# Performance work log

Measured on AMD Instinct MI355X. Metric: run time of the kernel, lower is better.

## Reference

```python
import jax, jax.numpy as jnp
import numpy as np

VOCAB = 65
N_EMBED = 384
BLOCK = 256
N_HEAD = 6
HEAD_SIZE = 4  # forward uses sa_heads = MultiHeadAttention(4), NOT the Block stack
B, T = 128, 256


def setup_inputs() -> dict:
    key = jax.random.key(0)
    ks = jax.random.split(key, 16)
    s = lambda *sh: 0.02
    inp = {
        "idx": jax.random.randint(ks[0], (B, T), 0, VOCAB),
        "targets": jax.random.randint(ks[1], (B, T), 0, VOCAB),
        "tok_emb": jax.random.normal(ks[2], (VOCAB, N_EMBED), jnp.float32) * 0.02,
        "pos_emb": jax.random.normal(ks[3], (BLOCK, N_EMBED), jnp.float32) * 0.02,
        "Wq": jax.random.normal(ks[4], (N_HEAD, N_EMBED, HEAD_SIZE), jnp.float32) * 0.05,
        "Wk": jax.random.normal(ks[5], (N_HEAD, N_EMBED, HEAD_SIZE), jnp.float32) * 0.05,
        "Wv": jax.random.normal(ks[6], (N_HEAD, N_EMBED, HEAD_SIZE), jnp.float32) * 0.05,
        "Wproj": jax.random.normal(ks[7], (N_HEAD * HEAD_SIZE, N_EMBED), jnp.float32) * 0.05,
        "bproj": jnp.zeros((N_EMBED,), jnp.float32),
        "W1": jax.random.normal(ks[8], (N_EMBED, 4 * N_EMBED), jnp.float32) * 0.02,
        "b1": jnp.zeros((4 * N_EMBED,), jnp.float32),
        "W2": jax.random.normal(ks[9], (4 * N_EMBED, N_EMBED), jnp.float32) * 0.02,
        "b2": jnp.zeros((N_EMBED,), jnp.float32),
        "Wlm": jax.random.normal(ks[10], (N_EMBED, VOCAB), jnp.float32) * 0.02,
        "blm": jnp.zeros((VOCAB,), jnp.float32),
    }
    return inp


def _forward(idx, targets, tok_emb, pos_emb, Wq, Wk, Wv, Wproj, bproj, W1, b1, W2, b2, Wlm, blm):
    Bb, Tt = idx.shape
    x = tok_emb[idx] + pos_emb[:Tt]  # [B,T,C]
    # multi-head attention (manual, causal). NOTE: source scales by n_embed**-0.5 (C of input), not head_size.
    q = jnp.einsum("btc,hcd->bhtd", x, Wq)
    k = jnp.einsum("btc,hcd->bhtd", x, Wk)
    v = jnp.einsum("btc,hcd->bhtd", x, Wv)
    scores = jnp.einsum("bhtd,bhsd->bhts", q, k) * (N_EMBED ** -0.5)
    causal = jnp.tril(jnp.ones((Tt, Tt), bool))
    scores = jnp.where(causal, scores, -jnp.inf)
    w = jax.nn.softmax(scores, axis=-1)  # dropout = identity in eval
    attn = jnp.einsum("bhts,bhsd->bhtd", w, v)
    attn = attn.transpose(0, 2, 1, 3).reshape(Bb, Tt, N_HEAD * HEAD_SIZE)
    x = attn @ Wproj + bproj
    # feed-forward
    x = jax.nn.relu(x @ W1 + b1) @ W2 + b2
    logits = x @ Wlm + blm  # [B,T,V]
    logits_flat = logits.reshape(Bb * Tt, VOCAB)
    t_flat = targets.reshape(Bb * Tt)
    logp = jax.nn.log_softmax(logits_flat, axis=-1)
    loss = -jnp.mean(jnp.take_along_axis(logp, t_flat[:, None], axis=1))
    return logits_flat, loss


def reference(idx, targets, tok_emb, pos_emb, Wq, Wk, Wv, Wproj, bproj, W1, b1, W2, b2, Wlm, blm):
    return _forward(idx, targets, tok_emb, pos_emb, Wq, Wk, Wv, Wproj, bproj, W1, b1, W2, b2, Wlm, blm)
```

## Files before the change

### kernel.cpp

```cpp
#include <hip/hip_runtime.h>
#include <hip/hip_bf16.h>
#include <math.h>

typedef __hip_bfloat16 bf16;
typedef __attribute__((ext_vector_type(8))) short bf16x8;
typedef __attribute__((ext_vector_type(4))) float f32x4;
typedef __attribute__((ext_vector_type(8))) int i32x8;
typedef __attribute__((ext_vector_type(4))) int i32x4;
typedef unsigned char u8;
typedef unsigned int u32;

#define T_SEQ   256
#define C_EMB   384
#define NH      6
#define HS      4
#define NB      128
#define NTOK    (NB * T_SEQ)
#define VOC     65
#define FFDIM   1536
#define QKVW    72
#define PROJK   32
#define XROWS   (VOC * T_SEQ)

#define X2_SCALE    128.0f
#define W1_SCALE    128.0f
#define FF1_DESCALE (1.0f / (128.0f * 128.0f))
#define H1_SCALE    512.0f
#define W2_SCALE    128.0f
#define FF2_DESCALE (1.0f / (512.0f * 128.0f))

__device__ __forceinline__ float bf2f(bf16 x) { return __bfloat162float(x); }
__device__ __forceinline__ bf16  f2b(float x) { return __float2bfloat16(x); }
__device__ __forceinline__ short f2s(float x) { bf16 b = __float2bfloat16(x); return *reinterpret_cast<short*>(&b); }
__device__ __forceinline__ u8 f2fp8(float x) {
    return (u8)(__builtin_amdgcn_cvt_pk_fp8_f32(x, x, 0, false) & 0xff);
}
__device__ __forceinline__ u32 pk4fp8(const float* w) {
    int p = __builtin_amdgcn_cvt_pk_fp8_f32(w[0], w[1], 0, false);
    p = __builtin_amdgcn_cvt_pk_fp8_f32(w[2], w[3], p, true);
    return (u32)p;
}

__device__ __forceinline__ void glds16(const void* g, void* l) {
    __builtin_amdgcn_global_load_lds((const __attribute__((address_space(1))) void*)g,
                                     (__attribute__((address_space(3))) void*)l, 16, 0, 0);
}

__global__ void pack_all_kernel(const float* __restrict__ Wq, const float* __restrict__ Wk,
                                const float* __restrict__ Wv, const float* __restrict__ Wlm,
                                const float* __restrict__ Wproj,
                                const float* __restrict__ W1, const float* __restrict__ W2,
                                const float* __restrict__ tok_emb, const float* __restrict__ pos_emb,
                                bf16* __restrict__ WqkvT, bf16* __restrict__ WlmT,
                                bf16* __restrict__ WprojT, u8* __restrict__ W1P,
                                u8* __restrict__ W2P, bf16* __restrict__ xtab,
                                float* __restrict__ lossbuf) {
    int blk = blockIdx.x;
    int t = threadIdx.x;
    if (blk == 0 && t == 0) { lossbuf[0] = 0.f; ((int*)lossbuf)[1] = 0; }
    if (blk < 128) {
        int n = blk;
        for (int c = t; c < C_EMB; c += 256) {
            float v = 0.f;
            if (n < QKVW) {
                int sel = n / 24, r = n % 24, h = r >> 2, d = r & 3;
                const float* W = (sel == 0) ? Wq : (sel == 1) ? Wk : Wv;
                v = W[(h * C_EMB + c) * HS + d];
            }
            WqkvT[(size_t)n * C_EMB + c] = f2b(v);
        }
    } else if (blk < 256) {
        int n = blk - 128;
        for (int c = t; c < C_EMB; c += 256)
            WlmT[(size_t)n * C_EMB + c] = f2b(n < VOC ? Wlm[(size_t)c * VOC + n] : 0.f);
    } else if (blk < 640) {
        int n = blk - 256;
        int k = t;
        if (k < PROJK)
            WprojT[(size_t)n * PROJK + k] = f2b(k < 24 ? Wproj[(size_t)k * C_EMB + n] : 0.f);
    } else if (blk < 640 + 288) {
        int fb = blk - 640;
        int n16 = fb / 3, kk = fb % 3;
        int b0 = t * 8;
        int l = b0 >> 5;
        int j0 = b0 & 31;
        int n = n16 * 16 + (l & 15);
        int kb = kk * 128 + (l >> 4) * 32 + j0;
        union { u8 b[8]; uint2 u; } pk;
        #pragma unroll
        for (int e = 0; e < 8; ++e)
            pk.b[e] = f2fp8(W1[(size_t)(kb + e) * FFDIM + n] * W1_SCALE);
        *(uint2*)&W1P[(size_t)fb * 2048 + b0] = pk.u;
    } else if (blk < 640 + 576) {
        int fb = blk - 640 - 288;
        int n16 = fb / 12, kc = fb % 12;
        int b0 = t * 8;
        int l = b0 >> 5;
        int j0 = b0 & 31;
        int n = n16 * 16 + (l & 15);
        int kb = kc * 128 + (l >> 4) * 32 + j0;
        union { u8 b[8]; uint2 u; } pk;
        #pragma unroll
        for (int e = 0; e < 8; ++e)
            pk.b[e] = f2fp8(W2[(size_t)(kb + e) * C_EMB + n] * W2_SCALE);
        *(uint2*)&W2P[(size_t)fb * 2048 + b0] = pk.u;
    } else {
        int base = (blk - (640 + 576)) * 4;
        for (int r = 0; r < 4; ++r) {
            int row = base + r;
            int id = row >> 8, tt = row & 255;
            const float* te = tok_emb + (size_t)id * C_EMB;
            const float* pe = pos_emb + (size_t)tt * C_EMB;
            bf16* dst = xtab + (size_t)row * C_EMB;
            for (int c = t; c < C_EMB; c += 256)
                dst[c] = f2b(te[c] + pe[c]);
        }
    }
}

__global__ __launch_bounds__(512)
void qkv_gather_kernel(const int* __restrict__ idx, const bf16* __restrict__ xtab,
                       const bf16* __restrict__ Bt, float* __restrict__ outf) {
    __shared__ __align__(16) u8 As[16384];
    __shared__ __align__(16) u8 Bs[16384];
    __shared__ int rowid[128];
    int tid = threadIdx.x, lane = tid & 63, wave = tid >> 6;
    int bm = blockIdx.x * 128;
    int wm = (wave & 1) * 64, wn = (wave >> 1) * 32;
    int lrow = lane & 15, kq = lane >> 4;
    if (tid < 128) { int token = bm + tid; rowid[tid] = idx[token] * T_SEQ + (token & (T_SEQ - 1)); }
    __syncthreads();

    int r0 = tid >> 3;
    int s0 = (((tid & 7) * 16) - (r0 & 7) * 16) & 127;
    int c1 = tid + 512;
    int r1 = c1 >> 3;
    int s1 = (((c1 & 7) * 16) - (r1 & 7) * 16) & 127;
    const u8* xb = (const u8*)xtab;
    const u8* bb = (const u8*)Bt;
    long gA0 = (long)rowid[r0] * 768 + s0;
    long gA1 = (long)rowid[r1] * 768 + s1;
    long gB0 = (long)r0 * 768 + s0;
    long gB1 = (long)r1 * 768 + s1;
    int ro = (lrow & 7) * 16;

    f32x4 acc[4][2] = {};
    for (int k0 = 0; k0 < 768; k0 += 128) {
        glds16(xb + gA0 + k0, As + (size_t)tid * 16);
        glds16(xb + gA1 + k0, As + (size_t)c1 * 16);
        glds16(bb + gB0 + k0, Bs + (size_t)tid * 16);
        glds16(bb + gB1 + k0, Bs + (size_t)c1 * 16);
        __syncthreads();
        #pragma unroll
        for (int ks = 0; ks < 2; ++ks) {
            int off = (ks * 64 + kq * 16 + ro) & 127;
            bf16x8 af[4], bff[2];
            #pragma unroll
            for (int i = 0; i < 4; ++i)
                af[i] = *(const bf16x8*)&As[(size_t)(wm + i * 16 + lrow) * 128 + off];
            #pragma unroll
            for (int i = 0; i < 2; ++i)
                bff[i] = *(const bf16x8*)&Bs[(size_t)(wn + i * 16 + lrow) * 128 + off];
            #pragma unroll
            for (int mi = 0; mi < 4; ++mi)
                #pragma unroll
                for (int ni = 0; ni < 2; ++ni)
                    acc[mi][ni] = __builtin_amdgcn_mfma_f32_16x16x32_bf16(af[mi], bff[ni], acc[mi][ni], 0, 0, 0);
        }
        __syncthreads();
    }

    #pragma unroll
    for (int ni = 0; ni < 2; ++ni) {
        int col = wn + ni * 16 + lrow;
        if (col >= QKVW) continue;
        #pragma unroll
        for (int mi = 0; mi < 4; ++mi) {
            int orow = bm + wm + mi * 16 + kq * 4;
            #pragma unroll
            for (int r = 0; r < 4; ++r)
                outf[(size_t)(orow + r) * QKVW + col] = acc[mi][ni][r];
        }
    }
}

__global__ void attn_kernel(const float* __restrict__ qkv,
                            bf16* __restrict__ attnT) {
    int bh = blockIdx.x;
    int b = bh / NH, h = bh % NH;
    int t = threadIdx.x;
    __shared__ float4 kv[T_SEQ][2];
    const float* base = qkv + (size_t)(b * T_SEQ) * QKVW;
    kv[t][0] = *(const float4*)(base + t * QKVW + 24 + h * HS);
    kv[t][1] = *(const float4*)(base + t * QKVW + 48 + h * HS);
    __syncthreads();
    const float scale = 0.05103103630798288f;
    float4 q = *(const float4*)(base + t * QKVW + h * HS);
    float qx = q.x * scale, qy = q.y * scale, qz = q.z * scale, qw = q.w * scale;
    float sum0 = 0.f, sum1 = 0.f;
    float o0x = 0.f, o0y = 0.f, o0z = 0.f, o0w = 0.f;
    float o1x = 0.f, o1y = 0.f, o1z = 0.f, o1w = 0.f;
    int s = 0;
    for (; s + 1 <= t; s += 2) {
        float4 k0 = kv[s][0],     v0 = kv[s][1];
        float4 k1 = kv[s + 1][0], v1 = kv[s + 1][1];
        float p0 = __expf(qx * k0.x + qy * k0.y + qz * k0.z + qw * k0.w);
        float p1 = __expf(qx * k1.x + qy * k1.y + qz * k1.z + qw * k1.w);
        sum0 += p0; sum1 += p1;
        o0x += p0 * v0.x; o0y += p0 * v0.y; o0z += p0 * v0.z; o0w += p0 * v0.w;
        o1x += p1 * v1.x; o1y += p1 * v1.y; o1z += p1 * v1.z; o1w += p1 * v1.w;
    }
    if (s <= t) {
        float4 k0 = kv[s][0], v0 = kv[s][1];
        float p0 = __expf(qx * k0.x + qy * k0.y + qz * k0.z + qw * k0.w);
        sum0 += p0;
        o0x += p0 * v0.x; o0y += p0 * v0.y; o0z += p0 * v0.z; o0w += p0 * v0.w;
    }
    float inv = 1.f / (sum0 + sum1);
    bf16* out = attnT + (size_t)(b * T_SEQ + t) * PROJK + h * HS;
    out[0] = f2b((o0x + o1x) * inv);
    out[1] = f2b((o0y + o1y) * inv);
    out[2] = f2b((o0z + o1z) * inv);
    out[3] = f2b((o0w + o1w) * inv);
    if (h == 0) {
        bf16* pad = attnT + (size_t)(b * T_SEQ + t) * PROJK + 24;
        *(uint4*)pad = uint4{0, 0, 0, 0};
    }
}

__global__ __launch_bounds__(1024, 4)
void ff_mega_kernel(const bf16* __restrict__ attnT, const bf16* __restrict__ WprojT,
                    const float* __restrict__ bproj,
                    const u8* __restrict__ W1P, const float* __restrict__ b1,
                    const u8* __restrict__ W2P, const float* __restrict__ b2,
                    bf16* __restrict__ x3) {
    __shared__ __align__(16) u8 smem[98304];
    u8* x2_lds = smem;
    u8* h1t    = smem + 49152;
    short* As_p = (short*)(smem + 49152);
    short* Bs_p = (short*)(smem + 57344);

    int tid  = threadIdx.x;
    int lane = tid & 63;
    int wave = tid >> 6;
    int wrow = wave & 3;
    int wcol = wave >> 2;
    int bm   = blockIdx.x * 128;
    int lrow  = lane & 15;
    int khalf = lane >> 4;
    int wm  = wrow * 32;
    int wn6 = wcol * 96;
    int wn4 = wcol * 64;

    if (tid < 512) {
        int row = tid >> 2;
        int i0 = (tid & 3) * 16;
        int selem = ((i0 - ((row >> 1) & 3) * 16) & 63) >> 1;
        glds16(attnT + (size_t)(bm + row) * PROJK + selem, As_p + (size_t)tid * 8);
    }
    {
        int rowb = tid >> 2;
        int sel2 = (((tid & 3) * 16 - ((rowb >> 1) & 3) * 16) & 63) >> 1;
        glds16(WprojT + (size_t)rowb * PROJK + sel2, Bs_p + (size_t)tid * 8);
        int c = tid + 1024;
        if (c < 1536) {
            int rb = c >> 2;
            int s2 = (((c & 3) * 16 - ((rb >> 1) & 3) * 16) & 63) >> 1;
            glds16(WprojT + (size_t)rb * PROJK + s2, Bs_p + (size_t)c * 8);
        }
    }
    __syncthreads();

    f32x4 accp[2][6] = {};
    {
        int arot16 = ((lrow >> 1) & 3) * 16;
        int roff = ((khalf * 16 + arot16) & 63) >> 1;
        bf16x8 afp[2], bfp[6];
        #pragma unroll
        for (int i = 0; i < 2; ++i)
            afp[i] = *(const bf16x8*)&As_p[(size_t)(wm + i * 16 + lrow) * 32 + roff];
        #pragma unroll
        for (int i = 0; i < 6; ++i)
            bfp[i] = *(const bf16x8*)&Bs_p[(size_t)(wn6 + i * 16 + lrow) * 32 + roff];
        #pragma unroll
        for (int mi = 0; mi < 2; ++mi)
            #pragma unroll
            for (int ni = 0; ni < 6; ++ni)
                accp[mi][ni] = __builtin_amdgcn_mfma_f32_16x16x32_bf16(bfp[ni], afp[mi], accp[mi][ni], 0, 0, 0);
    }

    #pragma unroll
    for (int mi = 0; mi < 2; ++mi) {
        int m = wm + mi * 16 + lrow;
        #pragma unroll
        for (int ni = 0; ni < 6; ++ni) {
            int n0 = wn6 + ni * 16 + khalf * 4;
            float4 bv = *(const float4*)(bproj + n0);
            float w[4];
            w[0] = (accp[mi][ni][0] + bv.x) * X2_SCALE;
            w[1] = (accp[mi][ni][1] + bv.y) * X2_SCALE;
            w[2] = (accp[mi][ni][2] + bv.z) * X2_SCALE;
            w[3] = (accp[mi][ni][3] + bv.w) * X2_SCALE;
            *(u32*)&x2_lds[(size_t)(n0 >> 7) * 16384 + (size_t)m * 128 +
                           (((n0 & 127) + (m & 7) * 16) & 127)] = pk4fp8(w);
        }
    }
    __syncthreads();

    int arot8 = (lrow & 7) * 16;
    int off0 = (khalf * 32 + arot8) & 127;
    int off1 = (off0 + 16) & 127;

    f32x4 acc1[2][4] = {};
    f32x4 acc2[2][6] = {};

    for (int nt = 0; nt < 6; ++nt) {
        #pragma unroll
        for (int kk = 0; kk < 3; ++kk) {
            const u8* abase = x2_lds + (size_t)kk * 16384;
            i32x8 a[2];
            #pragma unroll
            for (int i = 0; i < 2; ++i) {
                const u8* rp = abase + (size_t)(wm + i * 16 + lrow) * 128;
                i32x4 lo = *(const i32x4*)(rp + off0);
                i32x4 hi = *(const i32x4*)(rp + off1);
                a[i][0]=lo[0]; a[i][1]=lo[1]; a[i][2]=lo[2]; a[i][3]=lo[3];
                a[i][4]=hi[0]; a[i][5]=hi[1]; a[i][6]=hi[2]; a[i][7]=hi[3];
            }
            const u8* wbase = W1P + ((size_t)((nt * 16 + wcol * 4) * 3 + kk)) * 2048
                                  + (size_t)lane * 32;
            #pragma unroll
            for (int j = 0; j < 4; ++j) {
                const u8* p = wbase + (size_t)j * 3 * 2048;
                i32x4 lo = *(const i32x4*)p;
                i32x4 hi = *(const i32x4*)(p + 16);
                i32x8 b;
                b[0]=lo[0]; b[1]=lo[1]; b[2]=lo[2]; b[3]=lo[3];
                b[4]=hi[0]; b[5]=hi[1]; b[6]=hi[2]; b[7]=hi[3];
                #pragma unroll
                for (int mi = 0; mi < 2; ++mi)
                    acc1[mi][j] = __builtin_amdgcn_mfma_scale_f32_16x16x128_f8f6f4(
                        b, a[mi], acc1[mi][j], 0, 0,
                        0, 0x7f7f7f7f, 0, 0x7f7f7f7f);
            }
        }

        #pragma unroll
        for (int mi = 0; mi < 2; ++mi) {
            int m = wm + mi * 16 + lrow;
            #pragma unroll
            for (int ni = 0; ni < 4; ++ni) {
                int n0 = wn4 + ni * 16 + khalf * 4;
                float4 bv = *(const float4*)(b1 + nt * 256 + n0);
                float w[4];
                w[0] = fmaxf(acc1[mi][ni][0] * FF1_DESCALE + bv.x, 0.f) * H1_SCALE;
                w[1] = fmaxf(acc1[mi][ni][1] * FF1_DESCALE + bv.y, 0.f) * H1_SCALE;
                w[2] = fmaxf(acc1[mi][ni][2] * FF1_DESCALE + bv.z, 0.f) * H1_SCALE;
                w[3] = fmaxf(acc1[mi][ni][3] * FF1_DESCALE + bv.w, 0.f) * H1_SCALE;
                *(u32*)&h1t[(size_t)m * 256 + ((n0 + (m & 7) * 16) & 255)] = pk4fp8(w);
                acc1[mi][ni] = f32x4{0.f, 0.f, 0.f, 0.f};
            }
        }
        __syncthreads();

        #pragma unroll
        for (int sk = 0; sk < 2; ++sk) {
            i32x8 a2[2];
            #pragma unroll
            for (int i = 0; i < 2; ++i) {
                const u8* rp = h1t + (size_t)(wm + i * 16 + lrow) * 256;
                int o0 = (sk * 128 + khalf * 32 + arot8) & 255;
                int o1 = (sk * 128 + khalf * 32 + 16 + arot8) & 255;
                i32x4 lo = *(const i32x4*)(rp + o0);
                i32x4 hi = *(const i32x4*)(rp + o1);
                a2[i][0]=lo[0]; a2[i][1]=lo[1]; a2[i][2]=lo[2]; a2[i][3]=lo[3];
                a2[i][4]=hi[0]; a2[i][5]=hi[1]; a2[i][6]=hi[2]; a2[i][7]=hi[3];
            }
            int kc = nt * 2 + sk;
            #pragma unroll
            for (int half = 0; half < 2; ++half) {
                #pragma unroll
                for (int j = 0; j < 3; ++j) {
                    int n16 = wcol * 6 + half * 3 + j;
                    const u8* p = W2P + ((size_t)n16 * 12 + kc) * 2048 + (size_t)lane * 32;
                    i32x4 lo = *(const i32x4*)p;
                    i32x4 hi = *(const i32x4*)(p + 16);
                    i32x8 bw;
                    bw[0]=lo[0]; bw[1]=lo[1]; bw[2]=lo[2]; bw[3]=lo[3];
                    bw[4]=hi[0]; bw[5]=hi[1]; bw[6]=hi[2]; bw[7]=hi[3];
                    #pragma unroll
                    for (int mi = 0; mi < 2; ++mi)
                        acc2[mi][half * 3 + j] = __builtin_amdgcn_mfma_scale_f32_16x16x128_f8f6f4(
                            bw, a2[mi], acc2[mi][half * 3 + j], 0, 0,
                            0, 0x7f7f7f7f, 0, 0x7f7f7f7f);
                }
            }
        }
        __syncthreads();
    }

    u8* Ep = smem;
    #pragma unroll
    for (int mi = 0; mi < 2; ++mi) {
        int m = wm + mi * 16 + lrow;
        #pragma unroll
        for (int ni = 0; ni < 6; ++ni) {
            int n0 = wn6 + ni * 16 + khalf * 4;
            float4 bv = *(const float4*)(b2 + n0);
            union { short s[4]; uint2 u; } pk;
            pk.s[0] = f2s(acc2[mi][ni][0] * FF2_DESCALE + bv.x);
            pk.s[1] = f2s(acc2[mi][ni][1] * FF2_DESCALE + bv.y);
            pk.s[2] = f2s(acc2[mi][ni][2] * FF2_DESCALE + bv.z);
            pk.s[3] = f2s(acc2[mi][ni][3] * FF2_DESCALE + bv.w);
            *(uint2*)&Ep[(size_t)m * 768 + ((n0 >> 7) << 8) +
                         ((((n0 & 127) * 2) + (m & 7) * 16) & 255)] = pk.u;
        }
    }
    __syncthreads();
    #pragma unroll
    for (int p = 0; p < 6; ++p) {
        int c = tid + p * 1024;
        int row = c / 48;
        int sl = c - row * 48;
        int g0 = sl * 16;
        int chunk = g0 >> 8;
        int loc = g0 & 255;
        uint4 v = *(const uint4*)&Ep[(size_t)row * 768 + (chunk << 8) +
                                     ((loc + (row & 7) * 16) & 255)];
        *(uint4*)((u8*)x3 + (size_t)(bm + row) * 768 + g0) = v;
    }
}

__global__ __launch_bounds__(512)
void lm_loss_kernel(const bf16* __restrict__ A, const bf16* __restrict__ Bt,
                    const float* __restrict__ bias, const int* __restrict__ targets,
                    float* __restrict__ outf, float* __restrict__ lossbuf,
                    float* __restrict__ out_loss, int M, int K) {
    __shared__ short As[128][32];
    __shared__ short Bs[128][32];
    __shared__ float Ls[128][66];
    __shared__ float red[128];
    int tid  = threadIdx.x;
    int lane = tid & 63;
    int wave = tid >> 6;
    int bm = blockIdx.x * 128;
    int wm = (wave & 1) * 64;
    int wn = (wave >> 1) * 32;
    int lrow  = lane & 15;
    int khalf = lane >> 4;

    int row = tid >> 2;
    int i0 = (tid & 3) * 16;
    int selem = ((i0 - ((row >> 1) & 3) * 16) & 63) >> 1;
    int arot = ((lrow >> 1) & 3) * 16;
    int roff = ((khalf * 16 + arot) & 63) >> 1;

    f32x4 acc[4][2] = {};
    for (int k0 = 0; k0 < K; k0 += 32) {
        glds16(A  + (size_t)(bm + row) * K + k0 + selem, (short*)As + (size_t)tid * 8);
        glds16(Bt + (size_t)row * K + k0 + selem,        (short*)Bs + (size_t)tid * 8);
        __syncthreads();

        bf16x8 af[4], bff[2];
        #pragma unroll
        for (int i = 0; i < 4; ++i)
            af[i] = *(const bf16x8*)&As[wm + i * 16 + lrow][roff];
        #pragma unroll
        for (int i = 0; i < 2; ++i)
            bff[i] = *(const bf16x8*)&Bs[wn + i * 16 + lrow][roff];
        #pragma unroll
        for (int mi = 0; mi < 4; ++mi)
            #pragma unroll
            for (int ni = 0; ni < 2; ++ni)
                acc[mi][ni] = __builtin_amdgcn_mfma_f32_16x16x32_bf16(af[mi], bff[ni], acc[mi][ni], 0, 0, 0);
        __syncthreads();
    }

    #pragma unroll
    for (int ni = 0; ni < 2; ++ni) {
        int col = wn + ni * 16 + lrow;
        if (col >= VOC) continue;
        float bv = bias[col];
        #pragma unroll
        for (int mi = 0; mi < 4; ++mi) {
            int lr = wm + mi * 16 + khalf * 4;
            #pragma unroll
            for (int r = 0; r < 4; ++r) {
                float v = acc[mi][ni][r] + bv;
                outf[(size_t)(bm + lr + r) * VOC + col] = v;
                Ls[lr + r][col] = v;
            }
        }
    }
    __syncthreads();

    if (tid < 128) {
        int token = bm + tid;
        int tgt = targets[token];
        float m = -1e30f, s = 0.f;
        #pragma unroll 8
        for (int c = 0; c < VOC; ++c) {
            float v = Ls[tid][c];
            float mn = fmaxf(m, v);
            s = s * __expf(m - mn) + __expf(v - mn);
            m = mn;
        }
        red[tid] = m + logf(s) - Ls[tid][tgt];
    }
    __syncthreads();
    if (tid < 64) {
        float s = red[tid] + red[tid + 64];
        #pragma unroll
        for (int off = 32; off > 0; off >>= 1) s += __shfl_xor(s, off);
        if (tid == 0) {
            atomicAdd(&lossbuf[0], s);
            __threadfence();
            int done = atomicAdd(&((int*)lossbuf)[1], 1);
            if (done == (NTOK / 128) - 1) {
                __threadfence();
                float total = atomicAdd(&lossbuf[0], 0.0f);
                out_loss[0] = total / (float)NTOK;
            }
        }
    }
}

extern "C" void kernel_launch(void* const* d_in, const int* in_sizes, int n_in,
                              void* d_out, int out_size, void* d_ws, size_t ws_size,
                              hipStream_t stream) {
    const int*   idx     = (const int*)  d_in[0];
    const int*   targets = (const int*)  d_in[1];
    const float* tok_emb = (const float*)d_in[2];
    const float* pos_emb = (const float*)d_in[3];
    const float* Wq      = (const float*)d_in[4];
    const float* Wk      = (const float*)d_in[5];
    const float* Wv      = (const float*)d_in[6];
    const float* Wproj   = (const float*)d_in[7];
    const float* bproj   = (const float*)d_in[8];
    const float* W1      = (const float*)d_in[9];
    const float* b1      = (const float*)d_in[10];
    const float* W2      = (const float*)d_in[11];
    const float* b2      = (const float*)d_in[12];
    const float* Wlm     = (const float*)d_in[13];
    const float* blm     = (const float*)d_in[14];

    char* ws = (char*)d_ws;
    bf16*  WprojT = (bf16*) (ws + 0);
    float* qkvbuf = (float*)(ws + 25165824);
    bf16*  attnT  = (bf16*) (ws + 34603008);
    bf16*  xtab   = (bf16*) (ws + 37748736);
    bf16*  x3     = (bf16*) (ws + 163577856);
    float* lossbuf= (float*)(ws + 188743680);
    u8*    W1P    = (u8*)   (ws + 188874752);
    u8*    W2P    = (u8*)   (ws + 190054400);
    bf16*  WqkvT  = (bf16*) (ws + 191234048);
    bf16*  WlmT   = (bf16*) (ws + 191332352);

    float* out_logits = (float*)d_out;
    float* out_loss   = out_logits + (size_t)NTOK * VOC;

    pack_all_kernel<<<640 + 576 + XROWS / 4, 256, 0, stream>>>(
        Wq, Wk, Wv, Wlm, Wproj, W1, W2, tok_emb, pos_emb,
        WqkvT, WlmT, WprojT, W1P, W2P, xtab, lossbuf);

    qkv_gather_kernel<<<NTOK / 128, 512, 0, stream>>>(idx, xtab, WqkvT, qkvbuf);
    attn_kernel<<<NB * NH, T_SEQ, 0, stream>>>(qkvbuf, attnT);

    ff_mega_kernel<<<NTOK / 128, 1024, 0, stream>>>(attnT, WprojT, bproj,
                                                    W1P, b1, W2P, b2, x3);

    lm_loss_kernel<<<NTOK / 128, 512, 0, stream>>>(x3, WlmT, blm, targets,
                                                   out_logits, lossbuf, out_loss, NTOK, C_EMB);
}
```

Measured before the change: 243.2 us.

## Halve row tiles in QKV and FF kernels, widen lm_loss K-tile

```diff
diff --git a/kernel.cpp b/kernel.cpp
--- a/kernel.cpp
+++ b/kernel.cpp
@@ -105,7 +105,7 @@
             pk.b[e] = f2fp8(W2[(size_t)(kb + e) * C_EMB + n] * W2_SCALE);
         *(uint2*)&W2P[(size_t)fb * 2048 + b0] = pk.u;
     } else {
-        int base = (blk - (640 + 576)) * 4;
+        int base = (blk - 1216) * 4;
         for (int r = 0; r < 4; ++r) {
             int row = base + r;
             int id = row >> 8, tt = row & 255;
@@ -121,14 +121,14 @@
 __global__ __launch_bounds__(512)
 void qkv_gather_kernel(const int* __restrict__ idx, const bf16* __restrict__ xtab,
                        const bf16* __restrict__ Bt, float* __restrict__ outf) {
-    __shared__ __align__(16) u8 As[16384];
+    __shared__ __align__(16) u8 As[8192];
     __shared__ __align__(16) u8 Bs[16384];
-    __shared__ int rowid[128];
+    __shared__ int rowid[64];
     int tid = threadIdx.x, lane = tid & 63, wave = tid >> 6;
-    int bm = blockIdx.x * 128;
-    int wm = (wave & 1) * 64, wn = (wave >> 1) * 32;
+    int bm = blockIdx.x * 64;
+    int wm = (wave & 1) * 32, wn = (wave >> 1) * 32;
     int lrow = lane & 15, kq = lane >> 4;
-    if (tid < 128) { int token = bm + tid; rowid[tid] = idx[token] * T_SEQ + (token & (T_SEQ - 1)); }
+    if (tid < 64) { int token = bm + tid; rowid[tid] = idx[token] * T_SEQ + (token & (T_SEQ - 1)); }
     __syncthreads();
 
     int r0 = tid >> 3;
@@ -139,30 +139,28 @@
     const u8* xb = (const u8*)xtab;
     const u8* bb = (const u8*)Bt;
     long gA0 = (long)rowid[r0] * 768 + s0;
-    long gA1 = (long)rowid[r1] * 768 + s1;
     long gB0 = (long)r0 * 768 + s0;
     long gB1 = (long)r1 * 768 + s1;
     int ro = (lrow & 7) * 16;
 
-    f32x4 acc[4][2] = {};
+    f32x4 acc[2][2] = {};
     for (int k0 = 0; k0 < 768; k0 += 128) {
         glds16(xb + gA0 + k0, As + (size_t)tid * 16);
-        glds16(xb + gA1 + k0, As + (size_t)c1 * 16);
         glds16(bb + gB0 + k0, Bs + (size_t)tid * 16);
         glds16(bb + gB1 + k0, Bs + (size_t)c1 * 16);
         __syncthreads();
         #pragma unroll
         for (int ks = 0; ks < 2; ++ks) {
             int off = (ks * 64 + kq * 16 + ro) & 127;
-            bf16x8 af[4], bff[2];
-            #pragma unroll
-            for (int i = 0; i < 4; ++i)
+            bf16x8 af[2], bff[2];
+            #pragma unroll
+            for (int i = 0; i < 2; ++i)
                 af[i] = *(const bf16x8*)&As[(size_t)(wm + i * 16 + lrow) * 128 + off];
             #pragma unroll
             for (int i = 0; i < 2; ++i)
                 bff[i] = *(const bf16x8*)&Bs[(size_t)(wn + i * 16 + lrow) * 128 + off];
             #pragma unroll
-            for (int mi = 0; mi < 4; ++mi)
+            for (int mi = 0; mi < 2; ++mi)
                 #pragma unroll
                 for (int ni = 0; ni < 2; ++ni)
                     acc[mi][ni] = __builtin_amdgcn_mfma_f32_16x16x32_bf16(af[mi], bff[ni], acc[mi][ni], 0, 0, 0);
@@ -175,7 +173,7 @@
         int col = wn + ni * 16 + lrow;
         if (col >= QKVW) continue;
         #pragma unroll
-        for (int mi = 0; mi < 4; ++mi) {
+        for (int mi = 0; mi < 2; ++mi) {
             int orow = bm + wm + mi * 16 + kq * 4;
             #pragma unroll
             for (int r = 0; r < 4; ++r)
@@ -228,81 +226,56 @@
     }
 }
 
-__global__ __launch_bounds__(1024, 4)
+__global__ __launch_bounds__(512, 4)
 void ff_mega_kernel(const bf16* __restrict__ attnT, const bf16* __restrict__ WprojT,
                     const float* __restrict__ bproj,
                     const u8* __restrict__ W1P, const float* __restrict__ b1,
                     const u8* __restrict__ W2P, const float* __restrict__ b2,
                     bf16* __restrict__ x3) {
-    __shared__ __align__(16) u8 smem[98304];
+    __shared__ __align__(16) u8 smem[49152];
     u8* x2_lds = smem;
-    u8* h1t    = smem + 49152;
-    short* As_p = (short*)(smem + 49152);
-    short* Bs_p = (short*)(smem + 57344);
+    u8* h1t    = smem + 24576;
 
     int tid  = threadIdx.x;
     int lane = tid & 63;
     int wave = tid >> 6;
-    int wrow = wave & 3;
-    int wcol = wave >> 2;
-    int bm   = blockIdx.x * 128;
+    int bm   = blockIdx.x * 64;
     int lrow  = lane & 15;
     int khalf = lane >> 4;
-    int wm  = wrow * 32;
-    int wn6 = wcol * 96;
-    int wn4 = wcol * 64;
-
-    if (tid < 512) {
-        int row = tid >> 2;
-        int i0 = (tid & 3) * 16;
-        int selem = ((i0 - ((row >> 1) & 3) * 16) & 63) >> 1;
-        glds16(attnT + (size_t)(bm + row) * PROJK + selem, As_p + (size_t)tid * 8);
-    }
-    {
-        int rowb = tid >> 2;
-        int sel2 = (((tid & 3) * 16 - ((rowb >> 1) & 3) * 16) & 63) >> 1;
-        glds16(WprojT + (size_t)rowb * PROJK + sel2, Bs_p + (size_t)tid * 8);
-        int c = tid + 1024;
-        if (c < 1536) {
-            int rb = c >> 2;
-            int s2 = (((c & 3) * 16 - ((rb >> 1) & 3) * 16) & 63) >> 1;
-            glds16(WprojT + (size_t)rb * PROJK + s2, Bs_p + (size_t)c * 8);
-        }
-    }
-    __syncthreads();
-
-    f32x4 accp[2][6] = {};
-    {
-        int arot16 = ((lrow >> 1) & 3) * 16;
-        int roff = ((khalf * 16 + arot16) & 63) >> 1;
-        bf16x8 afp[2], bfp[6];
+    int wmh = (wave & 1) * 32;
+    int wn6 = (wave >> 1) * 96;
+    int wc  = wave >> 1;
+
+    #pragma unroll
+    for (int ph = 0; ph < 2; ++ph) {
+        f32x4 accp[2][3] = {};
+        bf16x8 afp[2], bfp[3];
         #pragma unroll
         for (int i = 0; i < 2; ++i)
-            afp[i] = *(const bf16x8*)&As_p[(size_t)(wm + i * 16 + lrow) * 32 + roff];
-        #pragma unroll
-        for (int i = 0; i < 6; ++i)
-            bfp[i] = *(const bf16x8*)&Bs_p[(size_t)(wn6 + i * 16 + lrow) * 32 + roff];
+            afp[i] = *(const bf16x8*)&attnT[(size_t)(bm + wmh + i * 16 + lrow) * PROJK + khalf * 8];
+        #pragma unroll
+        for (int i = 0; i < 3; ++i)
+            bfp[i] = *(const bf16x8*)&WprojT[(size_t)(wn6 + (ph * 3 + i) * 16 + lrow) * PROJK + khalf * 8];
         #pragma unroll
         for (int mi = 0; mi < 2; ++mi)
             #pragma unroll
-            for (int ni = 0; ni < 6; ++ni)
+            for (int ni = 0; ni < 3; ++ni)
                 accp[mi][ni] = __builtin_amdgcn_mfma_f32_16x16x32_bf16(bfp[ni], afp[mi], accp[mi][ni], 0, 0, 0);
-    }
-
-    #pragma unroll
-    for (int mi = 0; mi < 2; ++mi) {
-        int m = wm + mi * 16 + lrow;
-        #pragma unroll
-        for (int ni = 0; ni < 6; ++ni) {
-            int n0 = wn6 + ni * 16 + khalf * 4;
-            float4 bv = *(const float4*)(bproj + n0);
-            float w[4];
-            w[0] = (accp[mi][ni][0] + bv.x) * X2_SCALE;
-            w[1] = (accp[mi][ni][1] + bv.y) * X2_SCALE;
-            w[2] = (accp[mi][ni][2] + bv.z) * X2_SCALE;
-            w[3] = (accp[mi][ni][3] + bv.w) * X2_SCALE;
-            *(u32*)&x2_lds[(size_t)(n0 >> 7) * 16384 + (size_t)m * 128 +
-                           (((n0 & 127) + (m & 7) * 16) & 127)] = pk4fp8(w);
+        #pragma unroll
+        for (int mi = 0; mi < 2; ++mi) {
+            int m = wmh + mi * 16 + lrow;
+            #pragma unroll
+            for (int ni = 0; ni < 3; ++ni) {
+                int n0 = wn6 + (ph * 3 + ni) * 16 + khalf * 4;
+                float4 bv = *(const float4*)(bproj + n0);
+                float w[4];
+                w[0] = (accp[mi][ni][0] + bv.x) * X2_SCALE;
+                w[1] = (accp[mi][ni][1] + bv.y) * X2_SCALE;
+                w[2] = (accp[mi][ni][2] + bv.z) * X2_SCALE;
+                w[3] = (accp[mi][ni][3] + bv.w) * X2_SCALE;
+                *(u32*)&x2_lds[(size_t)(n0 >> 7) * 8192 + (size_t)m * 128 +
+                               (((n0 & 127) + (m & 7) * 16) & 127)] = pk4fp8(w);
+            }
         }
     }
     __syncthreads();
@@ -311,23 +284,23 @@
     int off0 = (khalf * 32 + arot8) & 127;
     int off1 = (off0 + 16) & 127;
 
-    f32x4 acc1[2][4] = {};
     f32x4 acc2[2][6] = {};
 
     for (int nt = 0; nt < 6; ++nt) {
+        f32x4 acc1[2][4] = {};
         #pragma unroll
         for (int kk = 0; kk < 3; ++kk) {
-            const u8* abase = x2_lds + (size_t)kk * 16384;
+            const u8* abase = x2_lds + (size_t)kk * 8192;
             i32x8 a[2];
             #pragma unroll
             for (int i = 0; i < 2; ++i) {
-                const u8* rp = abase + (size_t)(wm + i * 16 + lrow) * 128;
+                const u8* rp = abase + (size_t)(wmh + i * 16 + lrow) * 128;
                 i32x4 lo = *(const i32x4*)(rp + off0);
                 i32x4 hi = *(const i32x4*)(rp + off1);
                 a[i][0]=lo[0]; a[i][1]=lo[1]; a[i][2]=lo[2]; a[i][3]=lo[3];
                 a[i][4]=hi[0]; a[i][5]=hi[1]; a[i][6]=hi[2]; a[i][7]=hi[3];
             }
-            const u8* wbase = W1P + ((size_t)((nt * 16 + wcol * 4) * 3 + kk)) * 2048
+            const u8* wbase = W1P + ((size_t)((nt * 16 + wc * 4) * 3 + kk)) * 2048
                                   + (size_t)lane * 32;
             #pragma unroll
             for (int j = 0; j < 4; ++j) {
@@ -347,10 +320,10 @@
 
         #pragma unroll
         for (int mi = 0; mi < 2; ++mi) {
-            int m = wm + mi * 16 + lrow;
+            int m = wmh + mi * 16 + lrow;
             #pragma unroll
             for (int ni = 0; ni < 4; ++ni) {
-                int n0 = wn4 + ni * 16 + khalf * 4;
+                int n0 = wc * 64 + ni * 16 + khalf * 4;
                 float4 bv = *(const float4*)(b1 + nt * 256 + n0);
                 float w[4];
                 w[0] = fmaxf(acc1[mi][ni][0] * FF1_DESCALE + bv.x, 0.f) * H1_SCALE;
@@ -358,7 +331,6 @@
                 w[2] = fmaxf(acc1[mi][ni][2] * FF1_DESCALE + bv.z, 0.f) * H1_SCALE;
                 w[3] = fmaxf(acc1[mi][ni][3] * FF1_DESCALE + bv.w, 0.f) * H1_SCALE;
                 *(u32*)&h1t[(size_t)m * 256 + ((n0 + (m & 7) * 16) & 255)] = pk4fp8(w);
-                acc1[mi][ni] = f32x4{0.f, 0.f, 0.f, 0.f};
             }
         }
         __syncthreads();
@@ -368,7 +340,7 @@
             i32x8 a2[2];
             #pragma unroll
             for (int i = 0; i < 2; ++i) {
-                const u8* rp = h1t + (size_t)(wm + i * 16 + lrow) * 256;
+                const u8* rp = h1t + (size_t)(wmh + i * 16 + lrow) * 256;
                 int o0 = (sk * 128 + khalf * 32 + arot8) & 255;
                 int o1 = (sk * 128 + khalf * 32 + 16 + arot8) & 255;
                 i32x4 lo = *(const i32x4*)(rp + o0);
@@ -381,7 +353,7 @@
             for (int half = 0; half < 2; ++half) {
                 #pragma unroll
                 for (int j = 0; j < 3; ++j) {
-                    int n16 = wcol * 6 + half * 3 + j;
+                    int n16 = (wave >> 1) * 6 + half * 3 + j;
                     const u8* p = W2P + ((size_t)n16 * 12 + kc) * 2048 + (size_t)lane * 32;
                     i32x4 lo = *(const i32x4*)p;
                     i32x4 hi = *(const i32x4*)(p + 16);
@@ -402,7 +374,7 @@
     u8* Ep = smem;
     #pragma unroll
     for (int mi = 0; mi < 2; ++mi) {
-        int m = wm + mi * 16 + lrow;
+        int m = wmh + mi * 16 + lrow;
         #pragma unroll
         for (int ni = 0; ni < 6; ++ni) {
             int n0 = wn6 + ni * 16 + khalf * 4;
@@ -419,7 +391,7 @@
     __syncthreads();
     #pragma unroll
     for (int p = 0; p < 6; ++p) {
-        int c = tid + p * 1024;
+        int c = tid + p * 512;
         int row = c / 48;
         int sl = c - row * 48;
         int g0 = sl * 16;
@@ -435,9 +407,9 @@
 void lm_loss_kernel(const bf16* __restrict__ A, const bf16* __restrict__ Bt,
                     const float* __restrict__ bias, const int* __restrict__ targets,
                     float* __restrict__ outf, float* __restrict__ lossbuf,
-                    float* __restrict__ out_loss, int M, int K) {
-    __shared__ short As[128][32];
-    __shared__ short Bs[128][32];
+                    float* __restrict__ out_loss) {
+    __shared__ __align__(16) u8 As[16384];
+    __shared__ __align__(16) u8 Bs[16384];
     __shared__ float Ls[128][66];
     __shared__ float red[128];
     int tid  = threadIdx.x;
@@ -449,30 +421,42 @@
     int lrow  = lane & 15;
     int khalf = lane >> 4;
 
-    int row = tid >> 2;
-    int i0 = (tid & 3) * 16;
-    int selem = ((i0 - ((row >> 1) & 3) * 16) & 63) >> 1;
-    int arot = ((lrow >> 1) & 3) * 16;
-    int roff = ((khalf * 16 + arot) & 63) >> 1;
+    int r0 = tid >> 3;
+    int s0 = (((tid & 7) * 16) - (r0 & 7) * 16) & 127;
+    int c1 = tid + 512;
+    int r1 = c1 >> 3;
+    int s1 = (((c1 & 7) * 16) - (r1 & 7) * 16) & 127;
+    const u8* ab = (const u8*)A;
+    const u8* bb = (const u8*)Bt;
+    long gA0 = (long)(bm + r0) * 768 + s0;
+    long gA1 = (long)(bm + r1) * 768 + s1;
+    long gB0 = (long)r0 * 768 + s0;
+    long gB1 = (long)r1 * 768 + s1;
+    int ro = (lrow & 7) * 16;
 
     f32x4 acc[4][2] = {};
-    for (int k0 = 0; k0 < K; k0 += 32) {
-        glds16(A  + (size_t)(bm + row) * K + k0 + selem, (short*)As + (size_t)tid * 8);
-        glds16(Bt + (size_t)row * K + k0 + selem,        (short*)Bs + (size_t)tid * 8);
+    for (int k0 = 0; k0 < 768; k0 += 128) {
+        glds16(ab + gA0 + k0, As + (size_t)tid * 16);
+        glds16(ab + gA1 + k0, As + (size_t)c1 * 16);
+        glds16(bb + gB0 + k0, Bs + (size_t)tid * 16);
+        glds16(bb + gB1 + k0, Bs + (size_t)c1 * 16);
         __syncthreads();
-
-        bf16x8 af[4], bff[2];
-        #pragma unroll
-        for (int i = 0; i < 4; ++i)
-            af[i] = *(const bf16x8*)&As[wm + i * 16 + lrow][roff];
-        #pragma unroll
-        for (int i = 0; i < 2; ++i)
-            bff[i] = *(const bf16x8*)&Bs[wn + i * 16 + lrow][roff];
-        #pragma unroll
-        for (int mi = 0; mi < 4; ++mi)
-            #pragma unroll
-            for (int ni = 0; ni < 2; ++ni)
-                acc[mi][ni] = __builtin_amdgcn_mfma_f32_16x16x32_bf16(af[mi], bff[ni], acc[mi][ni], 0, 0, 0);
+        #pragma unroll
+        for (int ks = 0; ks < 2; ++ks) {
+            int off = (ks * 64 + khalf * 16 + ro) & 127;
+            bf16x8 af[4], bff[2];
+            #pragma unroll
+            for (int i = 0; i < 4; ++i)
+                af[i] = *(const bf16x8*)&As[(size_t)(wm + i * 16 + lrow) * 128 + off];
+            #pragma unroll
+            for (int i = 0; i < 2; ++i)
+                bff[i] = *(const bf16x8*)&Bs[(size_t)(wn + i * 16 + lrow) * 128 + off];
+            #pragma unroll
+            for (int mi = 0; mi < 4; ++mi)
+                #pragma unroll
+                for (int ni = 0; ni < 2; ++ni)
+                    acc[mi][ni] = __builtin_amdgcn_mfma_f32_16x16x32_bf16(af[mi], bff[ni], acc[mi][ni], 0, 0, 0);
+        }
         __syncthreads();
     }
 
@@ -559,16 +543,16 @@
     float* out_logits = (float*)d_out;
     float* out_loss   = out_logits + (size_t)NTOK * VOC;
 
-    pack_all_kernel<<<640 + 576 + XROWS / 4, 256, 0, stream>>>(
+    pack_all_kernel<<<1216 + XROWS / 4, 256, 0, stream>>>(
         Wq, Wk, Wv, Wlm, Wproj, W1, W2, tok_emb, pos_emb,
         WqkvT, WlmT, WprojT, W1P, W2P, xtab, lossbuf);
 
-    qkv_gather_kernel<<<NTOK / 128, 512, 0, stream>>>(idx, xtab, WqkvT, qkvbuf);
+    qkv_gather_kernel<<<NTOK / 64, 512, 0, stream>>>(idx, xtab, WqkvT, qkvbuf);
     attn_kernel<<<NB * NH, T_SEQ, 0, stream>>>(qkvbuf, attnT);
 
-    ff_mega_kernel<<<NTOK / 128, 1024, 0, stream>>>(attnT, WprojT, bproj,
-                                                    W1P, b1, W2P, b2, x3);
+    ff_mega_kernel<<<NTOK / 64, 512, 0, stream>>>(attnT, WprojT, bproj,
+                                                  W1P, b1, W2P, b2, x3);
 
     lm_loss_kernel<<<NTOK / 128, 512, 0, stream>>>(x3, WlmT, blm, targets,
-                                                   out_logits, lossbuf, out_loss, NTOK, C_EMB);
-}
+                                                   out_logits, lossbuf, out_loss);
+}
```

New measurement: 233.0 us. -4.2%, faster.
